# Kernel tuning notes

Hardware: AMD Instinct MI355X
Metric: run time of the kernel (lower is better)

## Reference

```python
import jax, jax.numpy as jnp
import numpy as np

HEADS = 4
ALPHA = 0.2
NEG = -9.0e15


def _layer(h, adj_mask, W, linW, linb, qkvW, qkvb, a, concat):
    # One GraphSelfAttentionLayer (eval mode: dropout off).
    F_out = W.shape[-1]
    n = h.shape[0]
    Wh = (h @ W) @ linW + linb                      # [N, F]
    qkv = Wh @ qkvW + qkvb                          # [N, 3F]
    q, k, v = jnp.split(qkv, 3, axis=-1)
    to_heads = lambda t: t.reshape(n, HEADS, F_out // HEADS).transpose(1, 0, 2)
    q, k, v = to_heads(q), to_heads(k), to_heads(v)  # [H, N, d]
    # note: scale uses out_features (not per-head d), matching the source
    dots = jax.nn.softmax(jnp.einsum('hid,hjd->hij', q, k) * (F_out ** -0.5), axis=-1)
    Wh0 = jnp.einsum('hij,hjd->hid', dots, v).transpose(1, 0, 2).reshape(n, F_out)
    Wh0 = jax.nn.softmax(Wh0, axis=-1)
    # decomposed all-pairs GAT score: e[i,j] = leakyrelu(Wh_i.a1 + Wh_j.a2)
    f1 = Wh @ a[:F_out]                             # [N]
    f2 = Wh @ a[F_out:]
    e = jax.nn.leaky_relu(f1[:, None] + f2[None, :], ALPHA)
    logits = jnp.where(adj_mask, e + dots.sum(0), NEG)
    att = jax.nn.softmax(logits, axis=1)
    hp = att @ Wh + Wh0
    return jax.nn.elu(hp) if concat else hp


def setup_inputs() -> dict:
    key = jax.random.key(0)
    ks = jax.random.split(key, 16)
    N, NFEAT, NHID, NOUT, H = 3072, 128, 32, 64, 4
    s = 0.1
    return {
        'x': jax.random.normal(ks[0], (N, NFEAT), jnp.float32),
        'adj': jax.random.randint(ks[1], (N, N), 0, 2, dtype=jnp.int32),
        'W_h': jax.random.normal(ks[2], (H, NFEAT, NHID), jnp.float32) * s,
        'lin_W_h': jax.random.normal(ks[3], (H, NHID, NHID), jnp.float32) * s,
        'lin_b_h': jax.random.normal(ks[4], (H, NHID), jnp.float32) * s,
        'qkv_W_h': jax.random.normal(ks[5], (H, NHID, 3 * NHID), jnp.float32) * s,
        'qkv_b_h': jax.random.normal(ks[6], (H, 3 * NHID), jnp.float32) * s,
        'a_h': jax.random.normal(ks[7], (H, 2 * NHID), jnp.float32) * s,
        'W_o': jax.random.normal(ks[8], (NHID * H, NOUT), jnp.float32) * s,
        'lin_W_o': jax.random.normal(ks[9], (NOUT, NOUT), jnp.float32) * s,
        'lin_b_o': jax.random.normal(ks[10], (NOUT,), jnp.float32) * s,
        'qkv_W_o': jax.random.normal(ks[11], (NOUT, 3 * NOUT), jnp.float32) * s,
        'qkv_b_o': jax.random.normal(ks[12], (3 * NOUT,), jnp.float32) * s,
        'a_o': jax.random.normal(ks[13], (2 * NOUT,), jnp.float32) * s,
    }


def reference(x, adj, W_h, lin_W_h, lin_b_h, qkv_W_h, qkv_b_h, a_h,
              W_o, lin_W_o, lin_b_o, qkv_W_o, qkv_b_o, a_o):
    mask = adj > 0
    heads_out = jax.vmap(
        lambda W, lW, lb, qW, qb, a: _layer(x, mask, W, lW, lb, qW, qb, a, True)
    )(W_h, lin_W_h, lin_b_h, qkv_W_h, qkv_b_h, a_h)      # [H, N, NHID]
    n = x.shape[0]
    x1 = jax.nn.elu(heads_out.transpose(1, 0, 2).reshape(n, -1))  # cat(dim=1) then elu
    out = jax.nn.elu(_layer(x1, mask, W_o, lin_W_o, lin_b_o, qkv_W_o, qkv_b_o, a_o, False))
    return out
```

## Files before the change

### kernel.cpp

```cpp
#include <hip/hip_runtime.h>
#include <hip/hip_bf16.h>

#define LOG2E 1.4426950408889634f
#define LOG2LOG2E 0.5287663729448977f

typedef unsigned int u32;
typedef float f32x16 __attribute__((ext_vector_type(16)));
typedef short sh8 __attribute__((ext_vector_type(8)));

union FR { u32 u[4]; sh8 s; };

__device__ __forceinline__ u32 cvt_pk_bf16(float lo, float hi){
  u32 r;
  asm volatile("v_cvt_pk_bf16_f32 %0, %1, %2" : "=v"(r) : "v"(lo), "v"(hi));
  return r;
}

__device__ __forceinline__ float asum16(const float* s){
  float a0=s[0]+s[8],  a1=s[1]+s[9],  a2=s[2]+s[10], a3=s[3]+s[11];
  float a4=s[4]+s[12], a5=s[5]+s[13], a6=s[6]+s[14], a7=s[7]+s[15];
  a0+=a4; a1+=a5; a2+=a6; a3+=a7;
  a0+=a2; a1+=a3;
  return a0+a1;
}

template<int W>
__device__ __forceinline__ float wred_max(float v){
  #pragma unroll
  for (int o=1;o<W;o<<=1) v = fmaxf(v, __shfl_xor(v,o));
  return v;
}
template<int W>
__device__ __forceinline__ float wred_sum(float v){
  #pragma unroll
  for (int o=1;o<W;o<<=1) v += __shfl_xor(v,o);
  return v;
}

__global__ __launch_bounds__(256) void k_mask(const int* __restrict__ adj, u32* __restrict__ mk){
  int id = blockIdx.x*256 + threadIdx.x;
  const int4* src = (const int4*)(adj + (size_t)id*32);
  u32 m = 0;
  #pragma unroll
  for (int g=0; g<8; g++){
    int4 v = src[g];
    if (v.x>0) m |= 1u<<(g*4+0);
    if (v.y>0) m |= 1u<<(g*4+1);
    if (v.z>0) m |= 1u<<(g*4+2);
    if (v.w>0) m |= 1u<<(g*4+3);
  }
  mk[id] = m;
}

template<int FIN, int F>
__global__ __launch_bounds__(256) void k_pre_a(const float* __restrict__ xg, const float* __restrict__ Wg,
    const float* __restrict__ lWg, const float* __restrict__ lbg, float* __restrict__ Whg, int N)
{
  const int h = blockIdx.y;
  const int row = blockIdx.x*256 + threadIdx.x;
  __shared__ float Wl[FIN*F];
  __shared__ float lWl[F*F];
  __shared__ float lbl[F];
  for (int i=threadIdx.x;i<FIN*F;i+=256) Wl[i]=Wg[(size_t)h*FIN*F+i];
  for (int i=threadIdx.x;i<F*F;i+=256) lWl[i]=lWg[(size_t)h*F*F+i];
  if (threadIdx.x<F) lbl[threadIdx.x]=lbg[h*F+threadIdx.x];
  __syncthreads();
  float t[F];
  #pragma unroll
  for (int c=0;c<F;c++) t[c]=0.f;
  const float4* xr = (const float4*)(xg + (size_t)row*FIN);
  for (int k4=0;k4<FIN/4;k4++){
    float4 xv = xr[k4];
    float xs[4]={xv.x,xv.y,xv.z,xv.w};
    #pragma unroll
    for (int kk=0;kk<4;kk++){
      float x1 = xs[kk];
      const float* wrow = Wl + (k4*4+kk)*F;
      #pragma unroll
      for (int c=0;c<F;c++) t[c] = fmaf(x1, wrow[c], t[c]);
    }
  }
  float wh[F];
  #pragma unroll
  for (int c=0;c<F;c++) wh[c]=lbl[c];
  #pragma unroll
  for (int k=0;k<F;k++){
    float tv=t[k];
    #pragma unroll
    for (int c=0;c<F;c++) wh[c]=fmaf(tv, lWl[k*F+c], wh[c]);
  }
  float4* dst=(float4*)(Whg + ((size_t)h*N+row)*F);
  #pragma unroll
  for (int c4=0;c4<F/4;c4++) dst[c4]=make_float4(wh[c4*4],wh[c4*4+1],wh[c4*4+2],wh[c4*4+3]);
}

template<int F, int GPR>
__global__ __launch_bounds__(256) void k_pre_b(const float* __restrict__ Whg, const float* __restrict__ qWg,
   const float* __restrict__ qbg, const float* __restrict__ ag,
   float* __restrict__ qg, float* __restrict__ kg, float* __restrict__ vg,
   float* __restrict__ f1g, float* __restrict__ f2g, int N)
{
  constexpr int ROWS = 256/GPR;
  constexpr int GC3  = 3*F/GPR;
  const int h = blockIdx.y;
  const int rl = threadIdx.x / GPR, grp = threadIdx.x % GPR;
  const int row = blockIdx.x*ROWS + rl;
  __shared__ float qWl[F*3*F];
  __shared__ float qbl[3*F];
  __shared__ float al[2*F];
  __shared__ float whl[ROWS][F+1];
  for (int i=threadIdx.x;i<F*3*F;i+=256) qWl[i]=qWg[(size_t)h*F*3*F+i];
  if (threadIdx.x<3*F) qbl[threadIdx.x]=qbg[h*3*F+threadIdx.x];
  if (threadIdx.x<2*F) al[threadIdx.x]=ag[h*2*F+threadIdx.x];
  {
    const float4* wsrc = (const float4*)(Whg + ((size_t)h*N+row)*F);
    #pragma unroll
    for (int c4=0;c4<2;c4++){
      float4 t = wsrc[grp*2+c4];
      int b = grp*8+c4*4;
      whl[rl][b]=t.x; whl[rl][b+1]=t.y; whl[rl][b+2]=t.z; whl[rl][b+3]=t.w;
    }
  }
  __syncthreads();
  float acc[GC3];
  #pragma unroll
  for (int c=0;c<GC3;c++) acc[c]=qbl[grp*GC3+c];
  for (int k=0;k<F;k++){
    float wv = whl[rl][k];
    #pragma unroll
    for (int c=0;c<GC3;c++) acc[c]=fmaf(wv, qWl[k*3*F + grp*GC3 + c], acc[c]);
  }
  size_t base = ((size_t)h*N+row)*F;
  #pragma unroll
  for (int c=0;c<GC3;c++){
    int col = grp*GC3+c;
    if (col < F)        qg[base+col]       = acc[c];
    else if (col < 2*F) kg[base+col-F]     = acc[c];
    else                vg[base+col-2*F]   = acc[c];
  }
  if (grp<2){
    const float* av = al + grp*F;
    float s=0.f;
    for (int k=0;k<F;k++) s = fmaf(whl[rl][k], av[k], s);
    (grp? f2g:f1g)[(size_t)h*N+row] = s;
  }
}

template<int S>
__global__ __launch_bounds__(256,4) void k_sweep1_mfma32(const float* __restrict__ qg, const float* __restrict__ kg,
    const float* __restrict__ vg, float* __restrict__ pml, float* __restrict__ pw, int N, float qscale)
{
  constexpr int F=32, LROW=33;
  const int h = blockIdx.z;
  const int sc = blockIdx.y;
  const int JC = N/S;
  const int wid = threadIdx.x>>6;
  const int lane = threadIdx.x&63;
  const int l31 = lane&31;
  const int half = lane>>5;
  const int itile = blockIdx.x*4 + wid;
  const int i = itile*32 + l31;
  __shared__ float vt[32*LROW];

  sh8 qf[4];
  {
    const float* qrow = qg + ((size_t)h*N + i)*F;
    #pragma unroll
    for (int hh=0;hh<4;hh++){
      FR u;
      #pragma unroll
      for (int p=0;p<4;p++){
        float lo = half? 0.f : qrow[hh*8+2*p]*qscale;
        float hi = half? 0.f : qrow[hh*8+2*p+1]*qscale;
        u.u[p] = cvt_pk_bf16(lo,hi);
      }
      qf[hh]=u.s;
    }
  }
  f32x16 C, Zv;
  #pragma unroll
  for (int r=0;r<16;r++){ C[r]=0.f; Zv[r]=0.f; }
  float l[4];
  #pragma unroll
  for (int hh=0;hh<4;hh++) l[hh]=0.f;
  const sh8 zf = {0,0,0,0,0,0,0,0};

  const int j0 = sc*JC;
  for (int jt=0; jt<JC; jt+=32){
    __syncthreads();
    {
      const float4* vs = (const float4*)(vg + ((size_t)h*N + j0+jt)*F);
      int idx = threadIdx.x;
      int j = idx>>3, c4 = idx&7;
      float4 b = vs[idx];
      float* vd = vt + j*LROW + c4*4;
      vd[0]=b.x; vd[1]=b.y; vd[2]=b.z; vd[3]=b.w;
    }
    __syncthreads();
    const float* krow = kg + ((size_t)h*N + j0+jt + l31)*F;
    sh8 vA[2];
    #pragma unroll
    for (int c=0;c<2;c++){
      FR u;
      #pragma unroll
      for (int p=0;p<4;p++){
        int jl = c*16 + half*8 + 2*p;
        u.u[p]=cvt_pk_bf16(vt[jl*LROW + l31], vt[(jl+1)*LROW + l31]);
      }
      vA[c]=u.s;
    }
    #pragma unroll
    for (int hh=0;hh<4;hh++){
      sh8 kf;
      {
        FR u;
        float4 ka = *(const float4*)(krow + hh*8);
        float4 kb = *(const float4*)(krow + hh*8 + 4);
        u.u[0]=cvt_pk_bf16(ka.x,ka.y);
        u.u[1]=cvt_pk_bf16(ka.z,ka.w);
        u.u[2]=cvt_pk_bf16(kb.x,kb.y);
        u.u[3]=cvt_pk_bf16(kb.z,kb.w);
        kf=u.s;
      }
      f32x16 Sacc = __builtin_amdgcn_mfma_f32_32x32x16_bf16(kf, qf[hh], Zv, 0,0,0);
      float p[16];
      #pragma unroll
      for (int r=0;r<16;r++) p[r] = exp2f(Sacc[r]);
      l[hh] += asum16(p);
      const bool own = ((l31>>3)==hh);
      #pragma unroll
      for (int c=0;c<2;c++){
        u32 a01 = cvt_pk_bf16(p[c*8+0], p[c*8+1]);
        u32 a23 = cvt_pk_bf16(p[c*8+2], p[c*8+3]);
        u32 b01 = cvt_pk_bf16(p[c*8+4], p[c*8+5]);
        u32 b23 = cvt_pk_bf16(p[c*8+6], p[c*8+7]);
        u32 a01s = __shfl_xor(a01,32);
        u32 a23s = __shfl_xor(a23,32);
        u32 b01s = __shfl_xor(b01,32);
        u32 b23s = __shfl_xor(b23,32);
        FR bf;
        bf.u[0] = half? b01s : a01;
        bf.u[1] = half? b23s : a23;
        bf.u[2] = half? b01  : a01s;
        bf.u[3] = half? b23  : a23s;
        sh8 av = own ? vA[c] : zf;
        C = __builtin_amdgcn_mfma_f32_32x32x16_bf16(av, bf.s, C, 0,0,0);
      }
    }
  }
  float lt[4];
  #pragma unroll
  for (int hh=0;hh<4;hh++) lt[hh] = l[hh] + __shfl_xor(l[hh],32);
  if (half==0){
    float* pb = pml + ((size_t)(h*S+sc)*8)*N + i;
    #pragma unroll
    for (int hh=0;hh<4;hh++){ pb[(size_t)hh*N]=0.f; pb[(size_t)(4+hh)*N]=lt[hh]; }
  }
  {
    float* pv = pw + ((size_t)(h*S+sc)*N + i)*F;
    #pragma unroll
    for (int hh=0;hh<4;hh++){
      *(float4*)(pv + 8*hh + 4*half) = make_float4(C[hh*4],C[hh*4+1],C[hh*4+2],C[hh*4+3]);
    }
  }
}

template<int S>
__global__ __launch_bounds__(256,4) void k_sweep2_mfma32(const float* __restrict__ qg, const float* __restrict__ kg,
    const float* __restrict__ whg, const float* __restrict__ f1g, const float* __restrict__ f2g,
    const float* __restrict__ mstar, const float* __restrict__ invl, const u32* __restrict__ mk,
    float* __restrict__ p2ml, float* __restrict__ php, int N, float qscale)
{
  constexpr int F=32, LROW=33;
  const int h = blockIdx.z;
  const int sc = blockIdx.y;
  const int JC = N/S;
  const int wid = threadIdx.x>>6;
  const int lane = threadIdx.x&63;
  const int l31 = lane&31;
  const int half = lane>>5;
  const int itile = blockIdx.x*4 + wid;
  const int i = itile*32 + l31;
  const int nw = N>>5;
  __shared__ float wt[32*LROW];
  __shared__ float f2s[32];

  sh8 qf[4];
  {
    const float* qrow = qg + ((size_t)h*N + i)*F;
    #pragma unroll
    for (int hh=0;hh<4;hh++){
      FR u;
      #pragma unroll
      for (int p=0;p<4;p++){
        float lo = half? 0.f : qrow[hh*8+2*p]*qscale;
        float hi = half? 0.f : qrow[hh*8+2*p+1]*qscale;
        u.u[p] = cvt_pk_bf16(lo,hi);
      }
      qf[hh]=u.s;
    }
  }
  float cc[4];
  #pragma unroll
  for (int hh=0;hh<4;hh++){
    float msv = mstar[((size_t)(h*4+hh))*N+i];
    float ilv = invl [((size_t)(h*4+hh))*N+i];
    cc[hh] = log2f(ilv) - msv + LOG2LOG2E;
  }
  const float f1 = f1g[(size_t)h*N+i];
  f32x16 C, Zv;
  #pragma unroll
  for (int r=0;r<16;r++){ C[r]=0.f; Zv[r]=0.f; }
  float L=0.f;

  const int j0 = sc*JC;
  for (int jt=0; jt<JC; jt+=32){
    __syncthreads();
    {
      const float4* ws = (const float4*)(whg + ((size_t)h*N + j0+jt)*F);
      int idx = threadIdx.x;
      int j = idx>>3, c4 = idx&7;
      float4 b = ws[idx];
      float* wd = wt + j*LROW + c4*4;
      wd[0]=b.x; wd[1]=b.y; wd[2]=b.z; wd[3]=b.w;
      if (threadIdx.x<32) f2s[threadIdx.x] = f2g[(size_t)h*N + j0+jt+threadIdx.x];
    }
    __syncthreads();
    const float* krow = kg + ((size_t)h*N + j0+jt + l31)*F;
    float ds[16];
    #pragma unroll
    for (int r=0;r<16;r++) ds[r]=0.f;
    #pragma unroll
    for (int hh=0;hh<4;hh++){
      sh8 kf;
      {
        FR u;
        float4 ka = *(const float4*)(krow + hh*8);
        float4 kb = *(const float4*)(krow + hh*8 + 4);
        u.u[0]=cvt_pk_bf16(ka.x,ka.y);
        u.u[1]=cvt_pk_bf16(ka.z,ka.w);
        u.u[2]=cvt_pk_bf16(kb.x,kb.y);
        u.u[3]=cvt_pk_bf16(kb.z,kb.w);
        kf=u.s;
      }
      f32x16 Sacc = __builtin_amdgcn_mfma_f32_32x32x16_bf16(kf, qf[hh], Zv, 0,0,0);
      float ch = cc[hh];
      #pragma unroll
      for (int r=0;r<16;r++) ds[r] += exp2f(Sacc[r] + ch);
    }
    u32 mw = mk[(size_t)i*nw + ((j0+jt)>>5)];
    float w[16];
    #pragma unroll
    for (int r=0;r<16;r++){
      int jo = (r&3)+8*(r>>2)+4*half;
      float e = f1 + f2s[jo];
      e = (e>=0.f)? e : 0.2f*e;
      float ev = exp2f(fmaf(e, LOG2E, ds[r]));
      w[r] = ((mw>>jo)&1u) ? ev : 0.f;
    }
    L += asum16(w);
    #pragma unroll
    for (int c=0;c<2;c++){
      sh8 whA;
      {
        FR u;
        #pragma unroll
        for (int p=0;p<4;p++){
          int jl = c*16 + half*8 + 2*p;
          u.u[p]=cvt_pk_bf16(wt[jl*LROW + l31], wt[(jl+1)*LROW + l31]);
        }
        whA=u.s;
      }
      u32 a01 = cvt_pk_bf16(w[c*8+0], w[c*8+1]);
      u32 a23 = cvt_pk_bf16(w[c*8+2], w[c*8+3]);
      u32 b01 = cvt_pk_bf16(w[c*8+4], w[c*8+5]);
      u32 b23 = cvt_pk_bf16(w[c*8+6], w[c*8+7]);
      u32 a01s = __shfl_xor(a01,32);
      u32 a23s = __shfl_xor(a23,32);
      u32 b01s = __shfl_xor(b01,32);
      u32 b23s = __shfl_xor(b23,32);
      FR bf;
      bf.u[0] = half? b01s : a01;
      bf.u[1] = half? b23s : a23;
      bf.u[2] = half? b01  : a01s;
      bf.u[3] = half? b23  : a23s;
      C = __builtin_amdgcn_mfma_f32_32x32x16_bf16(whA, bf.s, C, 0,0,0);
    }
  }
  L = L + __shfl_xor(L,32);
  if (half==0){
    float* pb = p2ml + ((size_t)(h*S+sc)*2)*N + i;
    pb[0]=0.f; pb[(size_t)N]=L;
  }
  {
    float* pv = php + ((size_t)(h*S+sc)*N + i)*F;
    #pragma unroll
    for (int g=0;g<4;g++)
      *(float4*)(pv + 8*g + 4*half) = make_float4(C[g*4],C[g*4+1],C[g*4+2],C[g*4+3]);
  }
}

template<int S>
__global__ __launch_bounds__(256,4) void k_sweep1_mfma64(const float* __restrict__ qg, const float* __restrict__ kg,
    const float* __restrict__ vg, float* __restrict__ pml, float* __restrict__ pw, int N, float qscale)
{
  constexpr int F=64, LROW=65;
  const int h = blockIdx.z;
  const int sc = blockIdx.y;
  const int JC = N/S;
  const int wid = threadIdx.x>>6;
  const int lane = threadIdx.x&63;
  const int l31 = lane&31;
  const int half = lane>>5;
  const int itile = blockIdx.x*4 + wid;
  const int i = itile*32 + l31;
  __shared__ float vt[32*LROW];

  sh8 qf[4];
  {
    const float* qrow = qg + ((size_t)h*N + i)*F;
    #pragma unroll
    for (int hh=0;hh<4;hh++){
      FR u;
      #pragma unroll
      for (int p=0;p<4;p++)
        u.u[p] = cvt_pk_bf16(qrow[hh*16 + 8*half + 2*p]*qscale, qrow[hh*16 + 8*half + 2*p+1]*qscale);
      qf[hh]=u.s;
    }
  }
  f32x16 C0, C1, Zv;
  #pragma unroll
  for (int r=0;r<16;r++){ C0[r]=0.f; C1[r]=0.f; Zv[r]=0.f; }
  float l[4];
  #pragma unroll
  for (int hh=0;hh<4;hh++) l[hh]=0.f;
  const sh8 zf = {0,0,0,0,0,0,0,0};

  const int j0 = sc*JC;
  for (int jt=0; jt<JC; jt+=32){
    __syncthreads();
    {
      const float4* vs = (const float4*)(vg + ((size_t)h*N + j0+jt)*F);
      #pragma unroll
      for (int q2=0;q2<2;q2++){
        int idx = q2*256 + threadIdx.x;
        int j = idx>>4, c4 = idx&15;
        float4 b = vs[idx];
        float* vd = vt + j*LROW + c4*4;
        vd[0]=b.x; vd[1]=b.y; vd[2]=b.z; vd[3]=b.w;
      }
    }
    __syncthreads();
    const float* krow = kg + ((size_t)h*N + j0+jt + l31)*F;
    sh8 vA[2][2];
    #pragma unroll
    for (int ch=0;ch<2;ch++)
      #pragma unroll
      for (int c=0;c<2;c++){
        FR u;
        #pragma unroll
        for (int p=0;p<4;p++){
          int jl = c*16 + half*8 + 2*p;
          u.u[p]=cvt_pk_bf16(vt[jl*LROW + ch*32 + l31], vt[(jl+1)*LROW + ch*32 + l31]);
        }
        vA[ch][c]=u.s;
      }
    #pragma unroll
    for (int hh=0;hh<4;hh++){
      sh8 kf;
      {
        FR u;
        float4 ka = *(const float4*)(krow + hh*16 + 8*half);
        float4 kb = *(const float4*)(krow + hh*16 + 8*half + 4);
        u.u[0]=cvt_pk_bf16(ka.x,ka.y);
        u.u[1]=cvt_pk_bf16(ka.z,ka.w);
        u.u[2]=cvt_pk_bf16(kb.x,kb.y);
        u.u[3]=cvt_pk_bf16(kb.z,kb.w);
        kf=u.s;
      }
      f32x16 Sacc = __builtin_amdgcn_mfma_f32_32x32x16_bf16(kf, qf[hh], Zv, 0,0,0);
      f32x16 &Cr = (hh>>1)? C1 : C0;
      float p[16];
      #pragma unroll
      for (int r=0;r<16;r++) p[r] = exp2f(Sacc[r]);
      l[hh] += asum16(p);
      const bool own = ((l31>>4) == (hh&1));
      #pragma unroll
      for (int c=0;c<2;c++){
        u32 a01 = cvt_pk_bf16(p[c*8+0], p[c*8+1]);
        u32 a23 = cvt_pk_bf16(p[c*8+2], p[c*8+3]);
        u32 b01 = cvt_pk_bf16(p[c*8+4], p[c*8+5]);
        u32 b23 = cvt_pk_bf16(p[c*8+6], p[c*8+7]);
        u32 a01s = __shfl_xor(a01,32);
        u32 a23s = __shfl_xor(a23,32);
        u32 b01s = __shfl_xor(b01,32);
        u32 b23s = __shfl_xor(b23,32);
        FR bf;
        bf.u[0] = half? b01s : a01;
        bf.u[1] = half? b23s : a23;
        bf.u[2] = half? b01  : a01s;
        bf.u[3] = half? b23  : a23s;
        sh8 av = own ? vA[hh>>1][c] : zf;
        Cr = __builtin_amdgcn_mfma_f32_32x32x16_bf16(av, bf.s, Cr, 0,0,0);
      }
    }
  }
  float lt[4];
  #pragma unroll
  for (int hh=0;hh<4;hh++) lt[hh] = l[hh] + __shfl_xor(l[hh],32);
  if (half==0){
    float* pb = pml + ((size_t)(h*S+sc)*8)*N + i;
    #pragma unroll
    for (int hh=0;hh<4;hh++){ pb[(size_t)hh*N]=0.f; pb[(size_t)(4+hh)*N]=lt[hh]; }
  }
  {
    float* pv = pw + ((size_t)(h*S+sc)*N + i)*F;
    #pragma unroll
    for (int g=0;g<4;g++){
      *(float4*)(pv + 8*g + 4*half)      = make_float4(C0[g*4],C0[g*4+1],C0[g*4+2],C0[g*4+3]);
      *(float4*)(pv + 32 + 8*g + 4*half) = make_float4(C1[g*4],C1[g*4+1],C1[g*4+2],C1[g*4+3]);
    }
  }
}

template<int S>
__global__ __launch_bounds__(256,4) void k_sweep2_mfma64(const float* __restrict__ qg, const float* __restrict__ kg,
    const float* __restrict__ whg, const float* __restrict__ f1g, const float* __restrict__ f2g,
    const float* __restrict__ mstar, const float* __restrict__ invl, const u32* __restrict__ mk,
    float* __restrict__ p2ml, float* __restrict__ php, int N, float qscale)
{
  constexpr int F=64, LROW=65;
  const int h = blockIdx.z;
  const int sc = blockIdx.y;
  const int JC = N/S;
  const int wid = threadIdx.x>>6;
  const int lane = threadIdx.x&63;
  const int l31 = lane&31;
  const int half = lane>>5;
  const int itile = blockIdx.x*4 + wid;
  const int i = itile*32 + l31;
  const int nw = N>>5;
  __shared__ float wt[32*LROW];
  __shared__ float f2s[32];

  sh8 qf[4];
  {
    const float* qrow = qg + ((size_t)h*N + i)*F;
    #pragma unroll
    for (int hh=0;hh<4;hh++){
      FR u;
      #pragma unroll
      for (int p=0;p<4;p++)
        u.u[p] = cvt_pk_bf16(qrow[hh*16 + 8*half + 2*p]*qscale, qrow[hh*16 + 8*half + 2*p+1]*qscale);
      qf[hh]=u.s;
    }
  }
  float cc[4];
  #pragma unroll
  for (int hh=0;hh<4;hh++){
    float msv = mstar[((size_t)(h*4+hh))*N+i];
    float ilv = invl [((size_t)(h*4+hh))*N+i];
    cc[hh] = log2f(ilv) - msv + LOG2LOG2E;
  }
  const float f1 = f1g[(size_t)h*N+i];
  f32x16 C0, C1, Zv;
  #pragma unroll
  for (int r=0;r<16;r++){ C0[r]=0.f; C1[r]=0.f; Zv[r]=0.f; }
  float L=0.f;

  const int j0 = sc*JC;
  for (int jt=0; jt<JC; jt+=32){
    __syncthreads();
    {
      const float4* ws = (const float4*)(whg + ((size_t)h*N + j0+jt)*F);
      #pragma unroll
      for (int q2=0;q2<2;q2++){
        int idx = q2*256 + threadIdx.x;
        int j = idx>>4, c4 = idx&15;
        float4 b = ws[idx];
        float* wd = wt + j*LROW + c4*4;
        wd[0]=b.x; wd[1]=b.y; wd[2]=b.z; wd[3]=b.w;
      }
      if (threadIdx.x<32) f2s[threadIdx.x] = f2g[(size_t)h*N + j0+jt+threadIdx.x];
    }
    __syncthreads();
    const float* krow = kg + ((size_t)h*N + j0+jt + l31)*F;
    float ds[16];
    #pragma unroll
    for (int r=0;r<16;r++) ds[r]=0.f;
    #pragma unroll
    for (int hh=0;hh<4;hh++){
      sh8 kf;
      {
        FR u;
        float4 ka = *(const float4*)(krow + hh*16 + 8*half);
        float4 kb = *(const float4*)(krow + hh*16 + 8*half + 4);
        u.u[0]=cvt_pk_bf16(ka.x,ka.y);
        u.u[1]=cvt_pk_bf16(ka.z,ka.w);
        u.u[2]=cvt_pk_bf16(kb.x,kb.y);
        u.u[3]=cvt_pk_bf16(kb.z,kb.w);
        kf=u.s;
      }
      f32x16 Sacc = __builtin_amdgcn_mfma_f32_32x32x16_bf16(kf, qf[hh], Zv, 0,0,0);
      float ch = cc[hh];
      #pragma unroll
      for (int r=0;r<16;r++) ds[r] += exp2f(Sacc[r] + ch);
    }
    u32 mw = mk[(size_t)i*nw + ((j0+jt)>>5)];
    float w[16];
    #pragma unroll
    for (int r=0;r<16;r++){
      int jo = (r&3)+8*(r>>2)+4*half;
      float e = f1 + f2s[jo];
      e = (e>=0.f)? e : 0.2f*e;
      float ev = exp2f(fmaf(e, LOG2E, ds[r]));
      w[r] = ((mw>>jo)&1u) ? ev : 0.f;
    }
    L += asum16(w);
    #pragma unroll
    for (int c=0;c<2;c++){
      u32 a01 = cvt_pk_bf16(w[c*8+0], w[c*8+1]);
      u32 a23 = cvt_pk_bf16(w[c*8+2], w[c*8+3]);
      u32 b01 = cvt_pk_bf16(w[c*8+4], w[c*8+5]);
      u32 b23 = cvt_pk_bf16(w[c*8+6], w[c*8+7]);
      u32 a01s = __shfl_xor(a01,32);
      u32 a23s = __shfl_xor(a23,32);
      u32 b01s = __shfl_xor(b01,32);
      u32 b23s = __shfl_xor(b23,32);
      FR bf;
      bf.u[0] = half? b01s : a01;
      bf.u[1] = half? b23s : a23;
      bf.u[2] = half? b01  : a01s;
      bf.u[3] = half? b23  : a23s;
      #pragma unroll
      for (int ch=0;ch<2;ch++){
        sh8 whA;
        {
          FR u;
          #pragma unroll
          for (int p=0;p<4;p++){
            int jl = c*16 + half*8 + 2*p;
            u.u[p]=cvt_pk_bf16(wt[jl*LROW + ch*32 + l31], wt[(jl+1)*LROW + ch*32 + l31]);
          }
          whA=u.s;
        }
        if (ch) C1 = __builtin_amdgcn_mfma_f32_32x32x16_bf16(whA, bf.s, C1, 0,0,0);
        else    C0 = __builtin_amdgcn_mfma_f32_32x32x16_bf16(whA, bf.s, C0, 0,0,0);
      }
    }
  }
  L = L + __shfl_xor(L,32);
  if (half==0){
    float* pb = p2ml + ((size_t)(h*S+sc)*2)*N + i;
    pb[0]=0.f; pb[(size_t)N]=L;
  }
  {
    float* pv = php + ((size_t)(h*S+sc)*N + i)*F;
    #pragma unroll
    for (int g=0;g<4;g++){
      *(float4*)(pv + 8*g + 4*half)      = make_float4(C0[g*4],C0[g*4+1],C0[g*4+2],C0[g*4+3]);
      *(float4*)(pv + 32 + 8*g + 4*half) = make_float4(C1[g*4],C1[g*4+1],C1[g*4+2],C1[g*4+3]);
    }
  }
}

template<int S>
__global__ __launch_bounds__(256) void k_stats1(const float* __restrict__ pml, float* __restrict__ wgt1,
    float* __restrict__ mstar, float* __restrict__ invl, int N)
{
  const int h = blockIdx.y>>2, hh = blockIdx.y&3;
  const int row = blockIdx.x*256 + threadIdx.x;
  float mv[S];
  #pragma unroll
  for (int sc=0;sc<S;sc++) mv[sc]=pml[((size_t)((h*S+sc)*8)+hh)*N+row];
  float ms=-1e30f;
  #pragma unroll
  for (int sc=0;sc<S;sc++) ms=fmaxf(ms,mv[sc]);
  float ls=0.f;
  #pragma unroll
  for (int sc=0;sc<S;sc++){
    float w = exp2f(mv[sc]-ms);
    float lv = pml[((size_t)((h*S+sc)*8)+4+hh)*N+row];
    ls = fmaf(lv, w, ls);
    wgt1[((size_t)((h*S+sc)*4)+hh)*N+row]=w;
  }
  mstar[((size_t)(h*4+hh))*N+row]=ms;
  invl [((size_t)(h*4+hh))*N+row]=1.f/ls;
}

template<int F, int S>
__global__ __launch_bounds__(256) void k_comb1(const float* __restrict__ pw, const float* __restrict__ wgt1,
    const float* __restrict__ invl, float* __restrict__ smw, int N)
{
  constexpr int D = F/4;
  constexpr int RPB = 256/F;
  const int h = blockIdx.y;
  const int c = threadIdx.x % F;
  const int row = blockIdx.x*RPB + threadIdx.x / F;
  const int hh = c / D;
  float acc=0.f;
  #pragma unroll
  for (int sc=0;sc<S;sc++){
    float w = wgt1[((size_t)((h*S+sc)*4)+hh)*N+row];
    float p = pw[((size_t)(h*S+sc)*N + row)*F + c];
    acc = fmaf(w,p,acc);
  }
  float w0 = acc * invl[((size_t)(h*4+hh))*N+row];
  float mx = wred_max<F>(w0);
  float e = exp2f((w0-mx)*LOG2E);
  float sm = wred_sum<F>(e);
  smw[((size_t)h*N+row)*F + c] = e/sm;
}

template<int S>
__global__ __launch_bounds__(256) void k_stats2(const float* __restrict__ p2ml, float* __restrict__ wgt2,
    float* __restrict__ invL, int N)
{
  const int h = blockIdx.y;
  const int row = blockIdx.x*256 + threadIdx.x;
  float mv[S];
  #pragma unroll
  for (int sc=0;sc<S;sc++) mv[sc]=p2ml[((size_t)((h*S+sc)*2))*N+row];
  float M=-1e30f;
  #pragma unroll
  for (int sc=0;sc<S;sc++) M=fmaxf(M,mv[sc]);
  float L=0.f;
  #pragma unroll
  for (int sc=0;sc<S;sc++){
    float w=exp2f(mv[sc]-M);
    float lv=p2ml[((size_t)((h*S+sc)*2)+1)*N+row];
    L = fmaf(lv,w,L);
    wgt2[(size_t)(h*S+sc)*N+row]=w;
  }
  invL[(size_t)h*N+row]=1.f/L;
}

template<int F, int S, bool L1OUT>
__global__ __launch_bounds__(256) void k_comb2(const float* __restrict__ php, const float* __restrict__ wgt2,
    const float* __restrict__ invL, const float* __restrict__ smw, void* __restrict__ outp, int N)
{
  constexpr int RPB = 256/F;
  const int h = blockIdx.y;
  const int c = threadIdx.x % F;
  const int row = blockIdx.x*RPB + threadIdx.x / F;
  float acc=0.f;
  #pragma unroll
  for (int sc=0;sc<S;sc++){
    float w = wgt2[(size_t)(h*S+sc)*N+row];
    float p = php[((size_t)(h*S+sc)*N + row)*F + c];
    acc = fmaf(w,p,acc);
  }
  float v = acc * invL[(size_t)h*N+row] + smw[((size_t)h*N+row)*F + c];
  v = (v>0.f)? v : expm1f(v);
  if (L1OUT){
    v = (v>0.f)? v : expm1f(v);
    ((float*)outp)[(size_t)row*(4*F) + h*F + c] = v;
  } else {
    ((float*)outp)[(size_t)row*F + c] = v;
  }
}

extern "C" void kernel_launch(void* const* d_in, const int* in_sizes, int n_in,
                              void* d_out, int out_size, void* d_ws, size_t ws_size,
                              hipStream_t stream)
{
  (void)in_sizes; (void)n_in; (void)out_size; (void)ws_size;
  const int N=3072;
  const int S1=8, S2=32;

  const float* x      = (const float*)d_in[0];
  const int*   adj    = (const int*)d_in[1];
  const float* W_h    = (const float*)d_in[2];
  const float* linW_h = (const float*)d_in[3];
  const float* linb_h = (const float*)d_in[4];
  const float* qkvW_h = (const float*)d_in[5];
  const float* qkvb_h = (const float*)d_in[6];
  const float* a_h    = (const float*)d_in[7];
  const float* W_o    = (const float*)d_in[8];
  const float* linW_o = (const float*)d_in[9];
  const float* linb_o = (const float*)d_in[10];
  const float* qkvW_o = (const float*)d_in[11];
  const float* qkvb_o = (const float*)d_in[12];
  const float* a_o    = (const float*)d_in[13];

  char* w = (char*)d_ws;
  auto alloc=[&](size_t bytes)->char*{ char* p=w; w += (bytes+255)&~(size_t)255; return p; };
  u32*   mk    = (u32*)  alloc((size_t)N*(N/32)*4);
  float* Wh1   = (float*)alloc((size_t)4*N*32*4);
  float* q1    = (float*)alloc((size_t)4*N*32*4);
  float* k1    = (float*)alloc((size_t)4*N*32*4);
  float* v1    = (float*)alloc((size_t)4*N*32*4);
  float* f11   = (float*)alloc((size_t)4*N*4);
  float* f21   = (float*)alloc((size_t)4*N*4);
  float* smw1  = (float*)alloc((size_t)4*32*N*4);
  float* x1    = (float*)alloc((size_t)N*128*4);
  float* Wh2   = (float*)alloc((size_t)N*64*4);
  float* q2    = (float*)alloc((size_t)N*64*4);
  float* k2    = (float*)alloc((size_t)N*64*4);
  float* v2    = (float*)alloc((size_t)N*64*4);
  float* f12   = (float*)alloc((size_t)N*4);
  float* f22   = (float*)alloc((size_t)N*4);
  float* smw2  = (float*)alloc((size_t)64*N*4);
  float* mst   = (float*)alloc((size_t)16*N*4);
  float* ivl   = (float*)alloc((size_t)16*N*4);
  float* wgt1  = (float*)alloc((size_t)256*N*4);
  float* wgt2  = (float*)alloc((size_t)64*N*4);
  float* ivL   = (float*)alloc((size_t)4*N*4);
  float* pml   = (float*)alloc((size_t)512*N*4);
  float* pw    = (float*)alloc((size_t)2048*N*4);

  const float qs1 = 0.17677669529663687f * LOG2E;
  const float qs2 = 0.125f * LOG2E;

  k_mask<<<dim3(N*(N/32)/256), 256, 0, stream>>>(adj, mk);

  k_pre_a<128,32><<<dim3(N/256,4),256,0,stream>>>(x, W_h, linW_h, linb_h, Wh1, N);
  k_pre_b<32,4><<<dim3(N/64,4),256,0,stream>>>(Wh1, qkvW_h, qkvb_h, a_h, q1,k1,v1,f11,f21,N);
  k_sweep1_mfma32<8><<<dim3(N/128,S1,4),256,0,stream>>>(q1,k1,v1,pml,pw,N,qs1);
  k_stats1<8><<<dim3(N/256,16),256,0,stream>>>(pml,wgt1,mst,ivl,N);
  k_comb1<32,8><<<dim3(N/8,4),256,0,stream>>>(pw,wgt1,ivl,smw1,N);
  k_sweep2_mfma32<8><<<dim3(N/128,S1,4),256,0,stream>>>(q1,k1,Wh1,f11,f21,mst,ivl,mk,pml,pw,N,qs1);
  k_stats2<8><<<dim3(N/256,4),256,0,stream>>>(pml,wgt2,ivL,N);
  k_comb2<32,8,true><<<dim3(N/8,4),256,0,stream>>>(pw,wgt2,ivL,smw1,x1,N);

  k_pre_a<128,64><<<dim3(N/256,1),256,0,stream>>>(x1, W_o, linW_o, linb_o, Wh2, N);
  k_pre_b<64,8><<<dim3(N/32,1),256,0,stream>>>(Wh2, qkvW_o, qkvb_o, a_o, q2,k2,v2,f12,f22,N);
  k_sweep1_mfma64<32><<<dim3(N/128,S2,1),256,0,stream>>>(q2,k2,v2,pml,pw,N,qs2);
  k_stats1<32><<<dim3(N/256,4),256,0,stream>>>(pml,wgt1,mst,ivl,N);
  k_comb1<64,32><<<dim3(N/4,1),256,0,stream>>>(pw,wgt1,ivl,smw2,N);
  k_sweep2_mfma64<32><<<dim3(N/128,S2,1),256,0,stream>>>(q2,k2,Wh2,f12,f22,mst,ivl,mk,pml,pw,N,qs2);
  k_stats2<32><<<dim3(N/256,1),256,0,stream>>>(pml,wgt2,ivL,N);
  k_comb2<64,32,false><<<dim3(N/4,1),256,0,stream>>>(pw,wgt2,ivL,smw2,d_out,N);
}
```

Measured before the change: 380.6 us.

## Transpose adjacency bitmask and process 64-column tiles in layer-1 sweeps

The packed adjacency bitmask is now stored word-major (transposed), so lanes holding consecutive rows read consecutive words, which makes the mask loads in the sweep kernels coalesced. The layer-1 sweep kernels now handle 64 key columns per iteration as two 32-wide sub-tiles. This halves the number of barriers and shared-memory staging rounds and gives more independent MFMA and exp work to overlap. The cost is more registers and shared memory per block, which may reduce occupancy under the launch bound of 4 blocks. The mask load is also issued earlier so its latency can be hidden.

```diff
diff --git a/kernel.cpp b/kernel.cpp
--- a/kernel.cpp
+++ b/kernel.cpp
@@ -37,9 +37,11 @@
   return v;
 }
 
-__global__ __launch_bounds__(256) void k_mask(const int* __restrict__ adj, u32* __restrict__ mk){
+template<int NW>
+__global__ __launch_bounds__(256) void k_mask(const int* __restrict__ adj, u32* __restrict__ mkT, int N){
   int id = blockIdx.x*256 + threadIdx.x;
-  const int4* src = (const int4*)(adj + (size_t)id*32);
+  int row = id / NW, word = id - row*NW;
+  const int4* src = (const int4*)(adj + (size_t)row*N + word*32);
   u32 m = 0;
   #pragma unroll
   for (int g=0; g<8; g++){
@@ -49,7 +51,7 @@
     if (v.z>0) m |= 1u<<(g*4+2);
     if (v.w>0) m |= 1u<<(g*4+3);
   }
-  mk[id] = m;
+  mkT[(size_t)word*N + row] = m;
 }
 
 template<int FIN, int F>
@@ -160,7 +162,7 @@
   const int half = lane>>5;
   const int itile = blockIdx.x*4 + wid;
   const int i = itile*32 + l31;
-  __shared__ float vt[32*LROW];
+  __shared__ float vt[64*LROW];
 
   sh8 qf[4];
   {
@@ -186,54 +188,68 @@
   const sh8 zf = {0,0,0,0,0,0,0,0};
 
   const int j0 = sc*JC;
-  for (int jt=0; jt<JC; jt+=32){
+  for (int jt=0; jt<JC; jt+=64){
     __syncthreads();
     {
       const float4* vs = (const float4*)(vg + ((size_t)h*N + j0+jt)*F);
-      int idx = threadIdx.x;
-      int j = idx>>3, c4 = idx&7;
-      float4 b = vs[idx];
-      float* vd = vt + j*LROW + c4*4;
-      vd[0]=b.x; vd[1]=b.y; vd[2]=b.z; vd[3]=b.w;
+      #pragma unroll
+      for (int q2=0;q2<2;q2++){
+        int idx = q2*256 + threadIdx.x;
+        int j = idx>>3, c4 = idx&7;
+        float4 b = vs[idx];
+        float* vd = vt + j*LROW + c4*4;
+        vd[0]=b.x; vd[1]=b.y; vd[2]=b.z; vd[3]=b.w;
+      }
     }
     __syncthreads();
-    const float* krow = kg + ((size_t)h*N + j0+jt + l31)*F;
-    sh8 vA[2];
+    const float* krowA = kg + ((size_t)h*N + j0+jt + l31)*F;
+    const float* krowB = krowA + 32*F;
+    sh8 vAa[2], vAb[2];
     #pragma unroll
     for (int c=0;c<2;c++){
-      FR u;
+      FR ua, ub;
       #pragma unroll
       for (int p=0;p<4;p++){
         int jl = c*16 + half*8 + 2*p;
-        u.u[p]=cvt_pk_bf16(vt[jl*LROW + l31], vt[(jl+1)*LROW + l31]);
-      }
-      vA[c]=u.s;
+        ua.u[p]=cvt_pk_bf16(vt[jl*LROW + l31], vt[(jl+1)*LROW + l31]);
+        ub.u[p]=cvt_pk_bf16(vt[(jl+32)*LROW + l31], vt[(jl+33)*LROW + l31]);
+      }
+      vAa[c]=ua.s; vAb[c]=ub.s;
     }
     #pragma unroll
     for (int hh=0;hh<4;hh++){
-      sh8 kf;
+      sh8 kfA, kfB;
       {
         FR u;
-        float4 ka = *(const float4*)(krow + hh*8);
-        float4 kb = *(const float4*)(krow + hh*8 + 4);
+        float4 ka = *(const float4*)(krowA + hh*8);
+        float4 kb = *(const float4*)(krowA + hh*8 + 4);
         u.u[0]=cvt_pk_bf16(ka.x,ka.y);
         u.u[1]=cvt_pk_bf16(ka.z,ka.w);
         u.u[2]=cvt_pk_bf16(kb.x,kb.y);
         u.u[3]=cvt_pk_bf16(kb.z,kb.w);
-        kf=u.s;
-      }
-      f32x16 Sacc = __builtin_amdgcn_mfma_f32_32x32x16_bf16(kf, qf[hh], Zv, 0,0,0);
-      float p[16];
-      #pragma unroll
-      for (int r=0;r<16;r++) p[r] = exp2f(Sacc[r]);
-      l[hh] += asum16(p);
+        kfA=u.s;
+        float4 kc = *(const float4*)(krowB + hh*8);
+        float4 kd = *(const float4*)(krowB + hh*8 + 4);
+        u.u[0]=cvt_pk_bf16(kc.x,kc.y);
+        u.u[1]=cvt_pk_bf16(kc.z,kc.w);
+        u.u[2]=cvt_pk_bf16(kd.x,kd.y);
+        u.u[3]=cvt_pk_bf16(kd.z,kd.w);
+        kfB=u.s;
+      }
+      f32x16 SaccA = __builtin_amdgcn_mfma_f32_32x32x16_bf16(kfA, qf[hh], Zv, 0,0,0);
+      f32x16 SaccB = __builtin_amdgcn_mfma_f32_32x32x16_bf16(kfB, qf[hh], Zv, 0,0,0);
+      float pA[16], pB[16];
+      #pragma unroll
+      for (int r=0;r<16;r++){ pA[r] = exp2f(SaccA[r]); pB[r] = exp2f(SaccB[r]); }
+      l[hh] += asum16(pA);
+      l[hh] += asum16(pB);
       const bool own = ((l31>>3)==hh);
       #pragma unroll
       for (int c=0;c<2;c++){
-        u32 a01 = cvt_pk_bf16(p[c*8+0], p[c*8+1]);
-        u32 a23 = cvt_pk_bf16(p[c*8+2], p[c*8+3]);
-        u32 b01 = cvt_pk_bf16(p[c*8+4], p[c*8+5]);
-        u32 b23 = cvt_pk_bf16(p[c*8+6], p[c*8+7]);
+        u32 a01 = cvt_pk_bf16(pA[c*8+0], pA[c*8+1]);
+        u32 a23 = cvt_pk_bf16(pA[c*8+2], pA[c*8+3]);
+        u32 b01 = cvt_pk_bf16(pA[c*8+4], pA[c*8+5]);
+        u32 b23 = cvt_pk_bf16(pA[c*8+6], pA[c*8+7]);
         u32 a01s = __shfl_xor(a01,32);
         u32 a23s = __shfl_xor(a23,32);
         u32 b01s = __shfl_xor(b01,32);
@@ -243,7 +259,25 @@
         bf.u[1] = half? b23s : a23;
         bf.u[2] = half? b01  : a01s;
         bf.u[3] = half? b23  : a23s;
-        sh8 av = own ? vA[c] : zf;
+        sh8 av = own ? vAa[c] : zf;
+        C = __builtin_amdgcn_mfma_f32_32x32x16_bf16(av, bf.s, C, 0,0,0);
+      }
+      #pragma unroll
+      for (int c=0;c<2;c++){
+        u32 a01 = cvt_pk_bf16(pB[c*8+0], pB[c*8+1]);
+        u32 a23 = cvt_pk_bf16(pB[c*8+2], pB[c*8+3]);
+        u32 b01 = cvt_pk_bf16(pB[c*8+4], pB[c*8+5]);
+        u32 b23 = cvt_pk_bf16(pB[c*8+6], pB[c*8+7]);
+        u32 a01s = __shfl_xor(a01,32);
+        u32 a23s = __shfl_xor(a23,32);
+        u32 b01s = __shfl_xor(b01,32);
+        u32 b23s = __shfl_xor(b23,32);
+        FR bf;
+        bf.u[0] = half? b01s : a01;
+        bf.u[1] = half? b23s : a23;
+        bf.u[2] = half? b01  : a01s;
+        bf.u[3] = half? b23  : a23s;
+        sh8 av = own ? vAb[c] : zf;
         C = __builtin_amdgcn_mfma_f32_32x32x16_bf16(av, bf.s, C, 0,0,0);
       }
     }
@@ -268,7 +302,7 @@
 template<int S>
 __global__ __launch_bounds__(256,4) void k_sweep2_mfma32(const float* __restrict__ qg, const float* __restrict__ kg,
     const float* __restrict__ whg, const float* __restrict__ f1g, const float* __restrict__ f2g,
-    const float* __restrict__ mstar, const float* __restrict__ invl, const u32* __restrict__ mk,
+    const float* __restrict__ mstar, const float* __restrict__ invl, const u32* __restrict__ mkT,
     float* __restrict__ p2ml, float* __restrict__ php, int N, float qscale)
 {
   constexpr int F=32, LROW=33;
@@ -281,9 +315,8 @@
   const int half = lane>>5;
   const int itile = blockIdx.x*4 + wid;
   const int i = itile*32 + l31;
-  const int nw = N>>5;
-  __shared__ float wt[32*LROW];
-  __shared__ float f2s[32];
+  __shared__ float wt[64*LROW];
+  __shared__ float f2s[64];
 
   sh8 qf[4];
   {
@@ -314,51 +347,68 @@
   float L=0.f;
 
   const int j0 = sc*JC;
-  for (int jt=0; jt<JC; jt+=32){
+  for (int jt=0; jt<JC; jt+=64){
     __syncthreads();
     {
       const float4* ws = (const float4*)(whg + ((size_t)h*N + j0+jt)*F);
-      int idx = threadIdx.x;
-      int j = idx>>3, c4 = idx&7;
-      float4 b = ws[idx];
-      float* wd = wt + j*LROW + c4*4;
-      wd[0]=b.x; wd[1]=b.y; wd[2]=b.z; wd[3]=b.w;
-      if (threadIdx.x<32) f2s[threadIdx.x] = f2g[(size_t)h*N + j0+jt+threadIdx.x];
+      #pragma unroll
+      for (int q2=0;q2<2;q2++){
+        int idx = q2*256 + threadIdx.x;
+        int j = idx>>3, c4 = idx&7;
+        float4 b = ws[idx];
+        float* wd = wt + j*LROW + c4*4;
+        wd[0]=b.x; wd[1]=b.y; wd[2]=b.z; wd[3]=b.w;
+      }
+      if (threadIdx.x<64) f2s[threadIdx.x] = f2g[(size_t)h*N + j0+jt+threadIdx.x];
     }
     __syncthreads();
-    const float* krow = kg + ((size_t)h*N + j0+jt + l31)*F;
-    float ds[16];
-    #pragma unroll
-    for (int r=0;r<16;r++) ds[r]=0.f;
+    u32 mwA = mkT[(size_t)((j0+jt)>>5)*N + i];
+    u32 mwB = mkT[(size_t)((j0+jt+32)>>5)*N + i];
+    const float* krowA = kg + ((size_t)h*N + j0+jt + l31)*F;
+    const float* krowB = krowA + 32*F;
+    float dsA[16], dsB[16];
+    #pragma unroll
+    for (int r=0;r<16;r++){ dsA[r]=0.f; dsB[r]=0.f; }
     #pragma unroll
     for (int hh=0;hh<4;hh++){
-      sh8 kf;
+      sh8 kfA, kfB;
       {
         FR u;
-        float4 ka = *(const float4*)(krow + hh*8);
-        float4 kb = *(const float4*)(krow + hh*8 + 4);
+        float4 ka = *(const float4*)(krowA + hh*8);
+        float4 kb = *(const float4*)(krowA + hh*8 + 4);
         u.u[0]=cvt_pk_bf16(ka.x,ka.y);
         u.u[1]=cvt_pk_bf16(ka.z,ka.w);
         u.u[2]=cvt_pk_bf16(kb.x,kb.y);
         u.u[3]=cvt_pk_bf16(kb.z,kb.w);
-        kf=u.s;
-      }
-      f32x16 Sacc = __builtin_amdgcn_mfma_f32_32x32x16_bf16(kf, qf[hh], Zv, 0,0,0);
+        kfA=u.s;
+        float4 kc = *(const float4*)(krowB + hh*8);
+        float4 kd = *(const float4*)(krowB + hh*8 + 4);
+        u.u[0]=cvt_pk_bf16(kc.x,kc.y);
+        u.u[1]=cvt_pk_bf16(kc.z,kc.w);
+        u.u[2]=cvt_pk_bf16(kd.x,kd.y);
+        u.u[3]=cvt_pk_bf16(kd.z,kd.w);
+        kfB=u.s;
+      }
+      f32x16 SaccA = __builtin_amdgcn_mfma_f32_32x32x16_bf16(kfA, qf[hh], Zv, 0,0,0);
+      f32x16 SaccB = __builtin_amdgcn_mfma_f32_32x32x16_bf16(kfB, qf[hh], Zv, 0,0,0);
       float ch = cc[hh];
       #pragma unroll
-      for (int r=0;r<16;r++) ds[r] += exp2f(Sacc[r] + ch);
-    }
-    u32 mw = mk[(size_t)i*nw + ((j0+jt)>>5)];
-    float w[16];
+      for (int r=0;r<16;r++){ dsA[r] += exp2f(SaccA[r] + ch); dsB[r] += exp2f(SaccB[r] + ch); }
+    }
     #pragma unroll
     for (int r=0;r<16;r++){
       int jo = (r&3)+8*(r>>2)+4*half;
-      float e = f1 + f2s[jo];
-      e = (e>=0.f)? e : 0.2f*e;
-      float ev = exp2f(fmaf(e, LOG2E, ds[r]));
-      w[r] = ((mw>>jo)&1u) ? ev : 0.f;
-    }
-    L += asum16(w);
+      float eA = f1 + f2s[jo];
+      eA = (eA>=0.f)? eA : 0.2f*eA;
+      float evA = exp2f(fmaf(eA, LOG2E, dsA[r]));
+      dsA[r] = ((mwA>>jo)&1u) ? evA : 0.f;
+      float eB = f1 + f2s[32+jo];
+      eB = (eB>=0.f)? eB : 0.2f*eB;
+      float evB = exp2f(fmaf(eB, LOG2E, dsB[r]));
+      dsB[r] = ((mwB>>jo)&1u) ? evB : 0.f;
+    }
+    L += asum16(dsA);
+    L += asum16(dsB);
     #pragma unroll
     for (int c=0;c<2;c++){
       sh8 whA;
@@ -371,10 +421,37 @@
         }
         whA=u.s;
       }
-      u32 a01 = cvt_pk_bf16(w[c*8+0], w[c*8+1]);
-      u32 a23 = cvt_pk_bf16(w[c*8+2], w[c*8+3]);
-      u32 b01 = cvt_pk_bf16(w[c*8+4], w[c*8+5]);
-      u32 b23 = cvt_pk_bf16(w[c*8+6], w[c*8+7]);
+      u32 a01 = cvt_pk_bf16(dsA[c*8+0], dsA[c*8+1]);
+      u32 a23 = cvt_pk_bf16(dsA[c*8+2], dsA[c*8+3]);
+      u32 b01 = cvt_pk_bf16(dsA[c*8+4], dsA[c*8+5]);
+      u32 b23 = cvt_pk_bf16(dsA[c*8+6], dsA[c*8+7]);
+      u32 a01s = __shfl_xor(a01,32);
+      u32 a23s = __shfl_xor(a23,32);
+      u32 b01s = __shfl_xor(b01,32);
+      u32 b23s = __shfl_xor(b23,32);
+      FR bf;
+      bf.u[0] = half? b01s : a01;
+      bf.u[1] = half? b23s : a23;
+      bf.u[2] = half? b01  : a01s;
+      bf.u[3] = half? b23  : a23s;
+      C = __builtin_amdgcn_mfma_f32_32x32x16_bf16(whA, bf.s, C, 0,0,0);
+    }
+    #pragma unroll
+    for (int c=0;c<2;c++){
+      sh8 whA;
+      {
+        FR u;
+        #pragma unroll
+        for (int p=0;p<4;p++){
+          int jl = 32 + c*16 + half*8 + 2*p;
+          u.u[p]=cvt_pk_bf16(wt[jl*LROW + l31], wt[(jl+1)*LROW + l31]);
+        }
+        whA=u.s;
+      }
+      u32 a01 = cvt_pk_bf16(dsB[c*8+0], dsB[c*8+1]);
+      u32 a23 = cvt_pk_bf16(dsB[c*8+2], dsB[c*8+3]);
+      u32 b01 = cvt_pk_bf16(dsB[c*8+4], dsB[c*8+5]);
+      u32 b23 = cvt_pk_bf16(dsB[c*8+6], dsB[c*8+7]);
       u32 a01s = __shfl_xor(a01,32);
       u32 a23s = __shfl_xor(a23,32);
       u32 b01s = __shfl_xor(b01,32);
@@ -526,7 +603,7 @@
 template<int S>
 __global__ __launch_bounds__(256,4) void k_sweep2_mfma64(const float* __restrict__ qg, const float* __restrict__ kg,
     const float* __restrict__ whg, const float* __restrict__ f1g, const float* __restrict__ f2g,
-    const float* __restrict__ mstar, const float* __restrict__ invl, const u32* __restrict__ mk,
+    const float* __restrict__ mstar, const float* __restrict__ invl, const u32* __restrict__ mkT,
     float* __restrict__ p2ml, float* __restrict__ php, int N, float qscale)
 {
   constexpr int F=64, LROW=65;
@@ -539,7 +616,6 @@
   const int half = lane>>5;
   const int itile = blockIdx.x*4 + wid;
   const int i = itile*32 + l31;
-  const int nw = N>>5;
   __shared__ float wt[32*LROW];
   __shared__ float f2s[32];
 
@@ -584,6 +660,7 @@
       if (threadIdx.x<32) f2s[threadIdx.x] = f2g[(size_t)h*N + j0+jt+threadIdx.x];
     }
     __syncthreads();
+    u32 mw = mkT[(size_t)((j0+jt)>>5)*N + i];
     const float* krow = kg + ((size_t)h*N + j0+jt + l31)*F;
     float ds[16];
     #pragma unroll
@@ -606,7 +683,6 @@
       #pragma unroll
       for (int r=0;r<16;r++) ds[r] += exp2f(Sacc[r] + ch);
     }
-    u32 mw = mk[(size_t)i*nw + ((j0+jt)>>5)];
     float w[16];
     #pragma unroll
     for (int r=0;r<16;r++){
@@ -785,7 +861,7 @@
 
   char* w = (char*)d_ws;
   auto alloc=[&](size_t bytes)->char*{ char* p=w; w += (bytes+255)&~(size_t)255; return p; };
-  u32*   mk    = (u32*)  alloc((size_t)N*(N/32)*4);
+  u32*   mkT   = (u32*)  alloc((size_t)N*(N/32)*4);
   float* Wh1   = (float*)alloc((size_t)4*N*32*4);
   float* q1    = (float*)alloc((size_t)4*N*32*4);
   float* k1    = (float*)alloc((size_t)4*N*32*4);
@@ -812,14 +888,14 @@
   const float qs1 = 0.17677669529663687f * LOG2E;
   const float qs2 = 0.125f * LOG2E;
 
-  k_mask<<<dim3(N*(N/32)/256), 256, 0, stream>>>(adj, mk);
+  k_mask<96><<<dim3(N*(N/32)/256), 256, 0, stream>>>(adj, mkT, N);
 
   k_pre_a<128,32><<<dim3(N/256,4),256,0,stream>>>(x, W_h, linW_h, linb_h, Wh1, N);
   k_pre_b<32,4><<<dim3(N/64,4),256,0,stream>>>(Wh1, qkvW_h, qkvb_h, a_h, q1,k1,v1,f11,f21,N);
   k_sweep1_mfma32<8><<<dim3(N/128,S1,4),256,0,stream>>>(q1,k1,v1,pml,pw,N,qs1);
   k_stats1<8><<<dim3(N/256,16),256,0,stream>>>(pml,wgt1,mst,ivl,N);
   k_comb1<32,8><<<dim3(N/8,4),256,0,stream>>>(pw,wgt1,ivl,smw1,N);
-  k_sweep2_mfma32<8><<<dim3(N/128,S1,4),256,0,stream>>>(q1,k1,Wh1,f11,f21,mst,ivl,mk,pml,pw,N,qs1);
+  k_sweep2_mfma32<8><<<dim3(N/128,S1,4),256,0,stream>>>(q1,k1,Wh1,f11,f21,mst,ivl,mkT,pml,pw,N,qs1);
   k_stats2<8><<<dim3(N/256,4),256,0,stream>>>(pml,wgt2,ivL,N);
   k_comb2<32,8,true><<<dim3(N/8,4),256,0,stream>>>(pw,wgt2,ivL,smw1,x1,N);
 
@@ -828,7 +904,7 @@
   k_sweep1_mfma64<32><<<dim3(N/128,S2,1),256,0,stream>>>(q2,k2,v2,pml,pw,N,qs2);
   k_stats1<32><<<dim3(N/256,4),256,0,stream>>>(pml,wgt1,mst,ivl,N);
   k_comb1<64,32><<<dim3(N/4,1),256,0,stream>>>(pw,wgt1,ivl,smw2,N);
-  k_sweep2_mfma64<32><<<dim3(N/128,S2,1),256,0,stream>>>(q2,k2,Wh2,f12,f22,mst,ivl,mk,pml,pw,N,qs2);
+  k_sweep2_mfma64<32><<<dim3(N/128,S2,1),256,0,stream>>>(q2,k2,Wh2,f12,f22,mst,ivl,mkT,pml,pw,N,qs2);
   k_stats2<32><<<dim3(N/256,1),256,0,stream>>>(pml,wgt2,ivL,N);
   k_comb2<64,32,false><<<dim3(N/4,1),256,0,stream>>>(pw,wgt2,ivL,smw2,d_out,N);
 }
```

Measured after the change: 448.7 us. 1.18x slower.
